# Performance work log

Hardware: AMD Instinct MI355X
Metric: run time of the kernel (lower is better)

Reference implementation:

```python
import jax, jax.numpy as jnp
import numpy as np

N_HEAD = 16
D_HEAD = 64
LN_EPS = 1e-5


def _layernorm(x, g, b):
    mu = jnp.mean(x, axis=-1, keepdims=True)
    var = jnp.mean((x - mu) ** 2, axis=-1, keepdims=True)
    return (x - mu) * jax.lax.rsqrt(var + LN_EPS) * g + b


def setup_inputs() -> dict:
    key = jax.random.key(0)
    ks = jax.random.split(key, 10)
    n_token, d_model, d_inner, n_layer = 32000, 1024, 4096, 6
    qlen, mlen, bsz = 512, 512, 4
    s = 0.02
    return {
        'data': jax.random.randint(ks[0], (qlen, bsz), 0, n_token),
        'mems': jax.random.normal(ks[1], (n_layer, mlen, bsz, d_model), jnp.float32) * s,
        'emb': jax.random.normal(ks[2], (n_token, d_model), jnp.float32) * s,
        'Wq': jax.random.normal(ks[3], (n_layer, d_model, N_HEAD * D_HEAD), jnp.float32) * s,
        'Wkv': jax.random.normal(ks[4], (n_layer, d_model, 2 * N_HEAD * D_HEAD), jnp.float32) * s,
        'Wo': jax.random.normal(ks[5], (n_layer, N_HEAD * D_HEAD, d_model), jnp.float32) * s,
        'ln1_g': jnp.ones((n_layer, d_model), jnp.float32),
        'ln1_b': jnp.zeros((n_layer, d_model), jnp.float32),
        'W1': jax.random.normal(ks[6], (n_layer, d_model, d_inner), jnp.float32) * s,
        'b1': jnp.zeros((n_layer, d_inner), jnp.float32),
        'W2': jax.random.normal(ks[7], (n_layer, d_inner, d_model), jnp.float32) * s,
        'b2': jnp.zeros((n_layer, d_model), jnp.float32),
        'ln2_g': jnp.ones((n_layer, d_model), jnp.float32),
        'ln2_b': jnp.zeros((n_layer, d_model), jnp.float32),
    }


def reference(data, mems, emb, Wq, Wkv, Wo, ln1_g, ln1_b, W1, b1, W2, b2, ln2_g, ln2_b):
    qlen, bsz = data.shape
    n_layer, _, d_model = Wo.shape
    mlen = mems.shape[1]
    klen = mlen + qlen
    scale = 1.0 / np.sqrt(D_HEAD)

    # AdaptiveEmbedding (div_val=1, d_proj==d_embed): lookup * sqrt(d_proj)
    word_emb = emb[data] * np.sqrt(d_model)  # [q, b, d]

    # sinusoidal positional embedding over klen (attn_type=2), last qlen slice
    inv_freq = 1.0 / (10000.0 ** (jnp.arange(0, d_model, 2, dtype=jnp.float32) / d_model))
    pos_seq = jnp.arange(klen - 1, -1, -1, dtype=jnp.float32)
    sinu = pos_seq[:, None] * inv_freq[None, :]
    pos_emb = jnp.concatenate([jnp.sin(sinu), jnp.cos(sinu)], axis=-1)  # [klen, d]
    h = word_emb + pos_emb[-qlen:, None, :]

    # causal mask including memory: True = masked
    mask = jnp.triu(jnp.ones((qlen, klen), dtype=bool), k=1 + mlen)

    for l in range(n_layer):
        c = jnp.concatenate([mems[l], h], axis=0)  # [klen, b, d]
        q = (h @ Wq[l]).reshape(qlen, bsz, N_HEAD, D_HEAD)
        kv = (c @ Wkv[l]).reshape(klen, bsz, N_HEAD, 2 * D_HEAD)
        k, v = kv[..., :D_HEAD], kv[..., D_HEAD:]
        score = jnp.einsum('ibnd,jbnd->ijbn', q, k) * scale  # [q, klen, b, n]
        score = jnp.where(mask[:, :, None, None], -jnp.inf, score)
        prob = jax.nn.softmax(score, axis=1)
        attn_vec = jnp.einsum('ijbn,jbnd->ibnd', prob, v).reshape(qlen, bsz, N_HEAD * D_HEAD)
        h = _layernorm(h + attn_vec @ Wo[l], ln1_g[l], ln1_b[l])  # post-LN
        ff = jax.nn.relu(h @ W1[l] + b1[l]) @ W2[l] + b2[l]
        h = _layernorm(h + ff, ln2_g[l], ln2_b[l])
    return h
```

## Files before the change

### kernel.cpp

```cpp
#include <hip/hip_runtime.h>

typedef unsigned short u16;
typedef unsigned int u32;
typedef __bf16 bf16x8 __attribute__((ext_vector_type(8)));
typedef float f32x4 __attribute__((ext_vector_type(4)));
typedef u16 u16x8 __attribute__((ext_vector_type(8)));
typedef u16 u16x4 __attribute__((ext_vector_type(4)));
typedef u32 u32x4 __attribute__((ext_vector_type(4)));

__device__ __forceinline__ u16 f2bf(float f){
  unsigned u = __float_as_uint(f);
  u += 0x7FFFu + ((u >> 16) & 1u);
  return (u16)(u >> 16);
}
__device__ __forceinline__ float bf2f(u16 u){
  return __uint_as_float((u32)u << 16);
}
__device__ __forceinline__ u32 pack2bf(float a, float b){
  return (u32)f2bf(a) | ((u32)f2bf(b) << 16);
}
__device__ __forceinline__ void gload16(const void* g, void* l){
  __builtin_amdgcn_global_load_lds(
      (const __attribute__((address_space(1))) void*)g,
      (__attribute__((address_space(3))) void*)l, 16, 0, 0);
}

__global__ __launch_bounds__(256) void conv_bf16_t(const float* __restrict__ src, u16* __restrict__ dst,
                                                   int K, int N, size_t dls, int drow0){
  __shared__ u16 s[64 * 68];
  size_t lo = (size_t)blockIdx.z * K * N;
  int n0 = blockIdx.x << 6, k0 = blockIdx.y << 6;
  int t = threadIdx.x;
#pragma unroll
  for (int p = 0; p < 4; ++p){
    int idx = p * 1024 + t * 4;
    int kl = idx >> 6, nl = idx & 63;
    f32x4 v = *(const f32x4*)(src + lo + (size_t)(k0 + kl) * N + n0 + nl);
#pragma unroll
    for (int j = 0; j < 4; ++j) s[(nl + j) * 68 + kl] = f2bf(v[j]);
  }
  __syncthreads();
  u16* db = dst + blockIdx.z * dls;
#pragma unroll
  for (int p = 0; p < 4; ++p){
    int idx = p * 1024 + t * 4;
    int nl = idx >> 6, kl = idx & 63;
    u16x4 o;
#pragma unroll
    for (int j = 0; j < 4; ++j) o[j] = s[nl * 68 + kl + j];
    *(u16x4*)(db + (size_t)(drow0 + n0 + nl) * K + k0 + kl) = o;
  }
}

__global__ __launch_bounds__(256) void conv_bf16(const float* __restrict__ src, u16* __restrict__ dst){
  size_t i = ((size_t)blockIdx.x * 256 + threadIdx.x) * 4;
  f32x4 v = *(const f32x4*)(src + i);
  u16x4 o;
#pragma unroll
  for (int j = 0; j < 4; ++j) o[j] = f2bf(v[j]);
  *(u16x4*)(dst + i) = o;
}

__global__ __launch_bounds__(256) void embed_k(const int* __restrict__ data, const float* __restrict__ emb,
                                               float* __restrict__ h, u16* __restrict__ hbf){
  int idx = blockIdx.x * 256 + threadIdx.x;
  int r = idx >> 10, d = idx & 1023;
  int i = r >> 2;
  int e = data[r];
  float val = emb[(size_t)e * 1024 + d] * 32.0f;
  float pos = (float)(511 - i);
  int t = d & 511;
  float freq = powf(10000.0f, -(float)t * (1.0f / 512.0f));
  float ang = pos * freq;
  val += (d < 512) ? sinf(ang) : cosf(ang);
  h[idx] = val;
  hbf[idx] = f2bf(val);
}

template<int BM>
__global__ __launch_bounds__(256) void gemm_bt(
    const u16* __restrict__ A, const u16* __restrict__ Bt,
    const float* __restrict__ bias, float* __restrict__ C, u16* __restrict__ Cbf,
    u16* __restrict__ Cpart, int M, int N, int K, int kchunk, int relu,
    size_t zA, size_t zB, size_t zC)
{
  constexpr int MFR = BM / 32;
  constexpr int ASZ = BM * 64, BSZ = 128 * 64;
  __shared__ __align__(16) u16 sA[2 * ASZ];
  __shared__ __align__(16) u16 sB[2 * BSZ];
  int tid = threadIdx.x, lane = tid & 63;
  int wr = (tid >> 7) & 1, wc = (tid >> 6) & 1;
  int m0 = blockIdx.y * BM, n0 = blockIdx.x << 7;
  int z = blockIdx.z;
  int kbeg = Cpart ? z * kchunk : 0;

  const u16* Ap = A + (size_t)z * zA;
  const u16* Bp = Bt + (size_t)z * zB;

  f32x4 acc[MFR][4];
#pragma unroll
  for (int i = 0; i < MFR; ++i)
#pragma unroll
    for (int j = 0; j < 4; ++j) acc[i][j] = (f32x4)(0.0f);

  int srow8 = tid >> 3;
  int gslot8 = ((tid & 7) ^ (srow8 & 7)) << 3;
  const u16* Ab = Ap + (size_t)(m0 + srow8) * K + kbeg + gslot8;
  const u16* Bb = Bp + (size_t)(n0 + srow8) * K + kbeg + gslot8;
  const size_t rstep32 = (size_t)K << 5;

  auto stage = [&](int buf, int k0){
#pragma unroll
    for (int p = 0; p < BM / 32; ++p)
      gload16(Ab + p * rstep32 + k0, (void*)&sA[buf * ASZ + p * 2048 + tid * 8]);
#pragma unroll
    for (int p = 0; p < 4; ++p)
      gload16(Bb + p * rstep32 + k0, (void*)&sB[buf * BSZ + p * 2048 + tid * 8]);
  };

  int r15 = lane & 15, g = lane >> 4;
  int s0 = g ^ (r15 & 7);
  const int o0 = s0 * 8, o1 = (s0 ^ 4) * 8;
  const int paBase = (wr * (BM / 2) + r15) * 64;
  const int pbBase = (wc * 64 + r15) * 64;

  int nk = kchunk >> 6;
  stage(0, 0);
  __syncthreads();
  for (int t = 0; t < nk; ++t){
    int cur = t & 1;
    if (t + 1 < nk) stage(cur ^ 1, (t + 1) << 6);
    const u16* pa = sA + cur * ASZ;
    const u16* pb = sB + cur * BSZ;
    bf16x8 af[MFR][2], bfv[4][2];
#pragma unroll
    for (int mi = 0; mi < MFR; ++mi){
      af[mi][0] = *(const bf16x8*)(pa + paBase + mi * 1024 + o0);
      af[mi][1] = *(const bf16x8*)(pa + paBase + mi * 1024 + o1);
    }
#pragma unroll
    for (int ni = 0; ni < 4; ++ni){
      bfv[ni][0] = *(const bf16x8*)(pb + pbBase + ni * 1024 + o0);
      bfv[ni][1] = *(const bf16x8*)(pb + pbBase + ni * 1024 + o1);
    }
#pragma unroll
    for (int kk = 0; kk < 2; ++kk)
#pragma unroll
      for (int mi = 0; mi < MFR; ++mi)
#pragma unroll
        for (int ni = 0; ni < 4; ++ni)
          acc[mi][ni] = __builtin_amdgcn_mfma_f32_16x16x32_bf16(af[mi][kk], bfv[ni][kk], acc[mi][ni], 0, 0, 0);
    __syncthreads();
  }

  int colf = lane & 15, rowf = (lane >> 4) << 2;
  if (Cpart){
    u16* dst = Cpart + (size_t)z * M * N;
#pragma unroll
    for (int ni = 0; ni < 4; ++ni){
      int cg = n0 + (wc << 6) + ni * 16 + colf;
#pragma unroll
      for (int mi = 0; mi < MFR; ++mi){
        int rg = m0 + wr * (BM / 2) + mi * 16 + rowf;
#pragma unroll
        for (int r = 0; r < 4; ++r)
          dst[(size_t)(rg + r) * N + cg] = f2bf(acc[mi][ni][r]);
      }
    }
  } else {
#pragma unroll
    for (int ni = 0; ni < 4; ++ni){
      int cg = n0 + (wc << 6) + ni * 16 + colf;
      float bv = bias ? bias[cg] : 0.0f;
#pragma unroll
      for (int mi = 0; mi < MFR; ++mi){
        int rg = m0 + wr * (BM / 2) + mi * 16 + rowf;
#pragma unroll
        for (int r = 0; r < 4; ++r){
          float val = acc[mi][ni][r] + bv;
          if (relu) val = fmaxf(val, 0.0f);
          size_t o = (size_t)(rg + r) * N + cg;
          if (C)   C[o]   = val;
          if (Cbf) (Cbf + (size_t)z * zC)[o] = f2bf(val);
        }
      }
    }
  }
}

__global__ __launch_bounds__(256) void vtrans(const u16* __restrict__ src, int sstride, int co,
                                              u16* __restrict__ dst, int jdst0,
                                              size_t zsrc, size_t zdst){
  __shared__ u16 s[64 * 68];
  int jt = blockIdx.x, bnp = blockIdx.y;
  int b = bnp >> 4, n = bnp & 15;
  int t = threadIdx.x;
  const u16* sp = src + blockIdx.z * zsrc;
  u16* dp = dst + blockIdx.z * zdst;
  int j0l = jt << 6;
#pragma unroll
  for (int rr = 0; rr < 16; ++rr){
    int idx = rr * 256 + t;
    int jl = idx >> 6, dd = idx & 63;
    s[jl * 68 + dd] = sp[(size_t)((j0l + jl) * 4 + b) * sstride + co + n * 128 + 64 + dd];
  }
  __syncthreads();
#pragma unroll
  for (int ww = 0; ww < 16; ++ww){
    int idx = ww * 256 + t;
    int dd = idx >> 6, jl = idx & 63;
    dp[((size_t)(bnp * 64 + dd) << 10) + jdst0 + j0l + jl] = s[jl * 68 + dd];
  }
}

__global__ __launch_bounds__(256) void attn_mfma_split(
    const u16* __restrict__ qkv, const u16* __restrict__ kvm,
    const u16* __restrict__ vtbf, u16* __restrict__ obuf, float* __restrict__ mlbuf)
{
  __shared__ __align__(16) u16 sK[2][64 * 64];
  __shared__ __align__(16) u16 sV[2][64 * 64];
  int tid = threadIdx.x, lane = tid & 63, wid = tid >> 6;
  int g = lane >> 4, t = lane & 15;
  int qt = blockIdx.x, bnp = blockIdx.y, half = blockIdx.z;
  int b = bnp >> 4, n = bnp & 15;
  int i0 = qt * 64 + wid * 16;
  int i = i0 + t;

  union Cvt { u32x4 u; bf16x8 v; };

  bf16x8 qfrag[2];
#pragma unroll
  for (int ks = 0; ks < 2; ++ks)
    qfrag[ks] = *(const bf16x8*)(qkv + (size_t)(i * 4 + b) * 3072 + n * 64 + ks * 32 + g * 8);

  f32x4 oacc[4];
#pragma unroll
  for (int df = 0; df < 4; ++df) oacc[df] = (f32x4)(0.0f);
  float mrun = -1e30f, lrun = 0.0f;

  const u16* kb2; size_t kst; int joff, kt0, kt1;
  if (half == 0){ kb2 = kvm + n * 128;        kst = 2048; joff = 0;   kt0 = 0; kt1 = 8; }
  else          { kb2 = qkv + 1024 + n * 128; kst = 3072; joff = 512; kt0 = 8; kt1 = qt + 9; }
  const u16* vb2 = vtbf + ((size_t)bnp << 16);

  int srow = tid >> 3;
  int gsl = ((tid & 7) ^ (srow & 7)) << 3;

  auto stageKV = [&](int buf, int kt){
    int j0 = kt << 6;
#pragma unroll
    for (int p = 0; p < 2; ++p){
      int jl = srow + p * 32;
      gload16(kb2 + (size_t)((j0 + jl - joff) * 4 + b) * kst + gsl, (void*)&sK[buf][p * 2048 + tid * 8]);
    }
#pragma unroll
    for (int p = 0; p < 2; ++p){
      int dl = srow + p * 32;
      gload16(vb2 + ((size_t)dl << 10) + j0 + gsl, (void*)&sV[buf][p * 2048 + tid * 8]);
    }
  };

  stageKV(0, kt0);
  __syncthreads();
  for (int kt = kt0; kt < kt1; ++kt){
    int cur = (kt - kt0) & 1;
    if (kt + 1 < kt1) stageKV(cur ^ 1, kt + 1);
    int j0 = kt << 6;
    f32x4 sacc[4];
#pragma unroll
    for (int jf = 0; jf < 4; ++jf) sacc[jf] = (f32x4)(0.0f);
#pragma unroll
    for (int ks = 0; ks < 2; ++ks){
      int sl = ((ks * 4 + g) ^ (t & 7)) * 8;
#pragma unroll
      for (int jf = 0; jf < 4; ++jf){
        bf16x8 kf = *(const bf16x8*)(&sK[cur][(jf * 16 + t) * 64 + sl]);
        sacc[jf] = __builtin_amdgcn_mfma_f32_16x16x32_bf16(kf, qfrag[ks], sacc[jf], 0, 0, 0);
      }
    }
    bool part = (half == 1) && (j0 + 63 > i0 + 512);
    float ps[4][4];
    float tmax = -1e30f;
#pragma unroll
    for (int jf = 0; jf < 4; ++jf)
#pragma unroll
      for (int r = 0; r < 4; ++r){
        float s = sacc[jf][r] * 0.125f;
        if (part && (j0 + jf * 16 + g * 4 + r > i + 512)) s = -1e30f;
        ps[jf][r] = s;
        tmax = fmaxf(tmax, s);
      }
    tmax = fmaxf(tmax, __shfl_xor(tmax, 16));
    tmax = fmaxf(tmax, __shfl_xor(tmax, 32));
    float mnew = fmaxf(mrun, tmax);
    float sc = __expf(mrun - mnew);
    mrun = mnew;
    lrun *= sc;
    u32 pk0[2], pk1[2], pk2[2], pk3[2];
    {
      float e0, e1, e2, e3;
#define DO_JF(PK, JF) \
      e0 = __expf(ps[JF][0] - mnew); e1 = __expf(ps[JF][1] - mnew); \
      e2 = __expf(ps[JF][2] - mnew); e3 = __expf(ps[JF][3] - mnew); \
      lrun += (e0 + e1) + (e2 + e3); \
      PK[0] = pack2bf(e0, e1); PK[1] = pack2bf(e2, e3);
      DO_JF(pk0, 0) DO_JF(pk1, 1) DO_JF(pk2, 2) DO_JF(pk3, 3)
#undef DO_JF
    }
#pragma unroll
    for (int df = 0; df < 4; ++df)
#pragma unroll
      for (int r = 0; r < 4; ++r) oacc[df][r] *= sc;

    int srcA = t + 16 * ((2 * g) & 3);
    int srcB = t + 16 * ((2 * g + 1) & 3);
    bool ghi = (g >= 2);
#pragma unroll
    for (int ks = 0; ks < 2; ++ks){
      u32 w0a, w1a, w2a, w3a, w0b, w1b, w2b, w3b;
      if (ks == 0){
        w0a = __shfl((int)pk0[0], srcA); w1a = __shfl((int)pk0[1], srcA);
        w2a = __shfl((int)pk0[0], srcB); w3a = __shfl((int)pk0[1], srcB);
        w0b = __shfl((int)pk1[0], srcA); w1b = __shfl((int)pk1[1], srcA);
        w2b = __shfl((int)pk1[0], srcB); w3b = __shfl((int)pk1[1], srcB);
      } else {
        w0a = __shfl((int)pk2[0], srcA); w1a = __shfl((int)pk2[1], srcA);
        w2a = __shfl((int)pk2[0], srcB); w3a = __shfl((int)pk2[1], srcB);
        w0b = __shfl((int)pk3[0], srcA); w1b = __shfl((int)pk3[1], srcA);
        w2b = __shfl((int)pk3[0], srcB); w3b = __shfl((int)pk3[1], srcB);
      }
      Cvt c;
      c.u[0] = ghi ? w0b : w0a;
      c.u[1] = ghi ? w1b : w1a;
      c.u[2] = ghi ? w2b : w2a;
      c.u[3] = ghi ? w3b : w3a;
      bf16x8 pf = c.v;
      int sl = ((ks * 4 + g) ^ (t & 7)) * 8;
#pragma unroll
      for (int df = 0; df < 4; ++df){
        bf16x8 vf = *(const bf16x8*)(&sV[cur][(df * 16 + t) * 64 + sl]);
        oacc[df] = __builtin_amdgcn_mfma_f32_16x16x32_bf16(vf, pf, oacc[df], 0, 0, 0);
      }
    }
    __syncthreads();
  }
  lrun += __shfl_xor(lrun, 16);
  lrun += __shfl_xor(lrun, 32);

  u16* orow = obuf + ((size_t)(half * 2048 + i * 4 + b) << 10) + n * 64;
#pragma unroll
  for (int df = 0; df < 4; ++df){
#pragma unroll
    for (int h = 0; h < 2; ++h){
      *(u32*)(orow + df * 16 + g * 4 + 2 * h) = pack2bf(oacc[df][2 * h], oacc[df][2 * h + 1]);
    }
  }
  if (g == 0){
    float* ml = mlbuf + (((size_t)(half * 2048 + i * 4 + b)) * 16 + n) * 2;
    ml[0] = mrun; ml[1] = lrun;
  }
}

__global__ __launch_bounds__(256) void attn_merge(const u16* __restrict__ obuf,
                                                  const float* __restrict__ mlbuf,
                                                  u16* __restrict__ attnbf){
  int r = blockIdx.x, tid = threadIdx.x;
  int d0 = tid * 4, n = tid >> 4;
  const float* ml0 = mlbuf + ((size_t)r * 16 + n) * 2;
  const float* ml1 = mlbuf + ((size_t)(2048 + r) * 16 + n) * 2;
  float m0 = ml0[0], l0 = ml0[1], m1 = ml1[0], l1 = ml1[1];
  float M = fmaxf(m0, m1);
  float w0 = __expf(m0 - M), w1 = __expf(m1 - M);
  float inv = 1.0f / (w0 * l0 + w1 * l1);
  u16x4 o0 = *(const u16x4*)(obuf + ((size_t)r << 10) + d0);
  u16x4 o1 = *(const u16x4*)(obuf + ((size_t)(2048 + r) << 10) + d0);
  u16x4 o;
#pragma unroll
  for (int j = 0; j < 4; ++j) o[j] = f2bf((w0 * bf2f(o0[j]) + w1 * bf2f(o1[j])) * inv);
  *(u16x4*)(attnbf + ((size_t)r << 10) + d0) = o;
}

__global__ __launch_bounds__(256) void ln_k(const float* __restrict__ res, const u16* __restrict__ parts,
                                            size_t pstride, int np, const float* __restrict__ bias,
                                            const float* __restrict__ g, const float* __restrict__ bta,
                                            float* hout, u16* __restrict__ hbf)
{
  int row = blockIdx.x, tid = threadIdx.x;
  int d0 = tid << 2;
  size_t ro = (size_t)row << 10;
  f32x4 v = *(const f32x4*)(res + ro + d0);
  if (bias){
    f32x4 bv = *(const f32x4*)(bias + d0);
#pragma unroll
    for (int j = 0; j < 4; ++j) v[j] += bv[j];
  }
  for (int p = 0; p < np; ++p){
    u16x4 pv = *(const u16x4*)(parts + p * pstride + ro + d0);
#pragma unroll
    for (int j = 0; j < 4; ++j) v[j] += bf2f(pv[j]);
  }
  float s = (v[0] + v[1]) + (v[2] + v[3]);
  float s2 = (v[0] * v[0] + v[1] * v[1]) + (v[2] * v[2] + v[3] * v[3]);
#pragma unroll
  for (int off = 32; off; off >>= 1){ s += __shfl_xor(s, off); s2 += __shfl_xor(s2, off); }
  __shared__ float ps[8];
  int wid = tid >> 6, lane = tid & 63;
  if (lane == 0){ ps[wid] = s; ps[wid + 4] = s2; }
  __syncthreads();
  s  = ps[0] + ps[1] + ps[2] + ps[3];
  s2 = ps[4] + ps[5] + ps[6] + ps[7];
  float mu = s * 0.0009765625f;
  float var = s2 * 0.0009765625f - mu * mu;
  float rstd = rsqrtf(var + 1e-5f);
  f32x4 gv = *(const f32x4*)(g + d0);
  f32x4 bt = *(const f32x4*)(bta + d0);
  f32x4 ho;
  u16x4 hb;
#pragma unroll
  for (int j = 0; j < 4; ++j){
    float tv = (v[j] - mu) * rstd * gv[j] + bt[j];
    ho[j] = tv; hb[j] = f2bf(tv);
  }
  *(f32x4*)(hout + ro + d0) = ho;
  *(u16x4*)(hbf + ro + d0) = hb;
}

__global__ __launch_bounds__(256) void copy_f32(const f32x4* __restrict__ src, f32x4* __restrict__ dst){
  size_t i = (size_t)blockIdx.x * 256 + threadIdx.x;
  dst[i] = src[i];
}

extern "C" void kernel_launch(void* const* d_in, const int* in_sizes, int n_in,
                              void* d_out, int out_size, void* d_ws, size_t ws_size,
                              hipStream_t stream)
{
  const int*   data = (const int*)  d_in[0];
  const float* mems = (const float*)d_in[1];
  const float* emb  = (const float*)d_in[2];
  const float* Wq   = (const float*)d_in[3];
  const float* Wkv  = (const float*)d_in[4];
  const float* Wo   = (const float*)d_in[5];
  const float* ln1g = (const float*)d_in[6];
  const float* ln1b = (const float*)d_in[7];
  const float* W1   = (const float*)d_in[8];
  const float* b1   = (const float*)d_in[9];
  const float* W2   = (const float*)d_in[10];
  const float* b2   = (const float*)d_in[11];
  const float* ln2g = (const float*)d_in[12];
  const float* ln2b = (const float*)d_in[13];
  float* out = (float*)d_out;

  char* ws = (char*)d_ws;
  size_t off = 0;
  auto alloc = [&](size_t bytes) -> char* {
    char* p = ws + off;
    off = (off + bytes + 255) & ~(size_t)255;
    return p;
  };

  u16*   wqkv_bf = (u16*) alloc((size_t)6 * 3072 * 1024 * 2);
  u16*   wo_bf   = (u16*) alloc((size_t)6 * 1024 * 1024 * 2);
  u16*   w1_bf   = (u16*) alloc((size_t)6 * 4096 * 1024 * 2);
  u16*   w2_bf   = (u16*) alloc((size_t)6 * 1024 * 4096 * 2);
  u16*   memsbf  = (u16*) alloc((size_t)6 * 2048 * 1024 * 2);
  u16*   kvmem   = (u16*) alloc((size_t)6 * 2048 * 2048 * 2);
  u16*   vtbf    = (u16*) alloc((size_t)6 * 64 * 64 * 1024 * 2);
  float* h       = (float*)alloc((size_t)2048 * 1024 * 4);
  u16*   hbf     = (u16*) alloc((size_t)2048 * 1024 * 2);
  u16*   qkv     = (u16*) alloc((size_t)2048 * 3072 * 2);
  u16*   attnbf  = (u16*) alloc((size_t)2048 * 1024 * 2);
  u16*   f1bf    = (u16*) alloc((size_t)2048 * 4096 * 2);
  float* pbuf    = (float*)alloc((size_t)4 * 2048 * 1024 * 4);
  float* mlbuf   = (float*)alloc((size_t)2 * 2048 * 16 * 2 * 4);
  u16*   pbf     = (u16*)pbuf;
  const size_t PS = (size_t)2048 * 1024;
  const size_t VTL = (size_t)64 * 64 * 1024;

  conv_bf16_t<<<dim3(16, 16, 6), 256, 0, stream>>>(Wq,  wqkv_bf, 1024, 1024, (size_t)3072 * 1024, 0);
  conv_bf16_t<<<dim3(32, 16, 6), 256, 0, stream>>>(Wkv, wqkv_bf, 1024, 2048, (size_t)3072 * 1024, 1024);
  conv_bf16_t<<<dim3(16, 16, 6), 256, 0, stream>>>(Wo,  wo_bf,   1024, 1024, (size_t)1024 * 1024, 0);
  conv_bf16_t<<<dim3(64, 16, 6), 256, 0, stream>>>(W1,  w1_bf,   1024, 4096, (size_t)4096 * 1024, 0);
  conv_bf16_t<<<dim3(16, 64, 6), 256, 0, stream>>>(W2,  w2_bf,   4096, 1024, (size_t)4096 * 1024, 0);
  conv_bf16<<<12288, 256, 0, stream>>>(mems, memsbf);
  embed_k<<<8192, 256, 0, stream>>>(data, emb, h, hbf);
  gemm_bt<128><<<dim3(16, 16, 6), 256, 0, stream>>>(memsbf, wqkv_bf + (size_t)1024 * 1024, nullptr,
      nullptr, kvmem, nullptr, 2048, 2048, 1024, 1024, 0,
      (size_t)2048 * 1024, (size_t)3072 * 1024, (size_t)2048 * 2048);
  vtrans<<<dim3(8, 64, 6), 256, 0, stream>>>(kvmem, 2048, 0, vtbf, 0, (size_t)2048 * 2048, VTL);

  for (int l = 0; l < 6; ++l){
    u16* kvm_l = kvmem + (size_t)l * 2048 * 2048;
    u16* vt_l  = vtbf + (size_t)l * VTL;
    gemm_bt<128><<<dim3(24, 16), 256, 0, stream>>>(hbf, wqkv_bf + (size_t)l * 3072 * 1024, nullptr,
        nullptr, qkv, nullptr, 2048, 3072, 1024, 1024, 0, 0, 0, 0);
    vtrans<<<dim3(8, 64), 256, 0, stream>>>(qkv, 3072, 1024, vt_l, 512, 0, 0);
    attn_mfma_split<<<dim3(8, 64, 2), 256, 0, stream>>>(qkv, kvm_l, vt_l, (u16*)pbuf, mlbuf);
    attn_merge<<<2048, 256, 0, stream>>>((const u16*)pbuf, mlbuf, attnbf);
    gemm_bt<64><<<dim3(8, 32, 2), 256, 0, stream>>>(attnbf, wo_bf + (size_t)l * 1024 * 1024, nullptr,
        nullptr, nullptr, pbf, 2048, 1024, 1024, 512, 0, 0, 0, 0);
    ln_k<<<2048, 256, 0, stream>>>(h, pbf, PS, 2, nullptr, ln1g + l * 1024, ln1b + l * 1024, h, hbf);
    gemm_bt<128><<<dim3(32, 16), 256, 0, stream>>>(hbf, w1_bf + (size_t)l * 4096 * 1024,
        b1 + (size_t)l * 4096, nullptr, f1bf, nullptr, 2048, 4096, 1024, 1024, 1, 0, 0, 0);
    gemm_bt<64><<<dim3(8, 32, 4), 256, 0, stream>>>(f1bf, w2_bf + (size_t)l * 4096 * 1024, nullptr,
        nullptr, nullptr, pbf, 2048, 1024, 4096, 1024, 0, 0, 0, 0);
    ln_k<<<2048, 256, 0, stream>>>(h, pbf, PS, 4, b2 + l * 1024, ln2g + l * 1024, ln2b + l * 1024, h, hbf);
  }
  copy_f32<<<2048, 256, 0, stream>>>((const f32x4*)h, (f32x4*)out);
}
```

Measured before the change: 1.189 ms.

## Unsplit attention into single pass and drop merge kernel; retile QKV GEMM

The attention kernel no longer splits the key range into a memory half and a current-segment half. Each block now walks all key tiles itself and normalizes the output directly, which removes the separate merge kernel and the intermediate partial-output and max/sum buffers. In exchange the grid halves to 512 blocks, so each block runs longer and fewer blocks are available to fill the GPU. The QKV projection GEMM also switches to the 64-row tile template with twice as many blocks.

```diff
diff --git a/kernel.cpp b/kernel.cpp
--- a/kernel.cpp
+++ b/kernel.cpp
@@ -213,15 +213,15 @@
   }
 }
 
-__global__ __launch_bounds__(256) void attn_mfma_split(
+__global__ __launch_bounds__(256) void attn_mfma(
     const u16* __restrict__ qkv, const u16* __restrict__ kvm,
-    const u16* __restrict__ vtbf, u16* __restrict__ obuf, float* __restrict__ mlbuf)
+    const u16* __restrict__ vtbf, u16* __restrict__ attnbf)
 {
   __shared__ __align__(16) u16 sK[2][64 * 64];
   __shared__ __align__(16) u16 sV[2][64 * 64];
   int tid = threadIdx.x, lane = tid & 63, wid = tid >> 6;
   int g = lane >> 4, t = lane & 15;
-  int qt = blockIdx.x, bnp = blockIdx.y, half = blockIdx.z;
+  int qt = blockIdx.x, bnp = blockIdx.y;
   int b = bnp >> 4, n = bnp & 15;
   int i0 = qt * 64 + wid * 16;
   int i = i0 + t;
@@ -238,9 +238,8 @@
   for (int df = 0; df < 4; ++df) oacc[df] = (f32x4)(0.0f);
   float mrun = -1e30f, lrun = 0.0f;
 
-  const u16* kb2; size_t kst; int joff, kt0, kt1;
-  if (half == 0){ kb2 = kvm + n * 128;        kst = 2048; joff = 0;   kt0 = 0; kt1 = 8; }
-  else          { kb2 = qkv + 1024 + n * 128; kst = 3072; joff = 512; kt0 = 8; kt1 = qt + 9; }
+  const u16* kbm = kvm + n * 128;
+  const u16* kbh = qkv + 1024 + n * 128;
   const u16* vb2 = vtbf + ((size_t)bnp << 16);
 
   int srow = tid >> 3;
@@ -248,10 +247,13 @@
 
   auto stageKV = [&](int buf, int kt){
     int j0 = kt << 6;
+    const u16* kb = (kt < 8) ? kbm : kbh;
+    size_t kst = (kt < 8) ? 2048 : 3072;
+    int joff = (kt < 8) ? 0 : 512;
 #pragma unroll
     for (int p = 0; p < 2; ++p){
       int jl = srow + p * 32;
-      gload16(kb2 + (size_t)((j0 + jl - joff) * 4 + b) * kst + gsl, (void*)&sK[buf][p * 2048 + tid * 8]);
+      gload16(kb + (size_t)((j0 + jl - joff) * 4 + b) * kst + gsl, (void*)&sK[buf][p * 2048 + tid * 8]);
     }
 #pragma unroll
     for (int p = 0; p < 2; ++p){
@@ -260,10 +262,11 @@
     }
   };
 
-  stageKV(0, kt0);
+  int kt1 = qt + 9;
+  stageKV(0, 0);
   __syncthreads();
-  for (int kt = kt0; kt < kt1; ++kt){
-    int cur = (kt - kt0) & 1;
+  for (int kt = 0; kt < kt1; ++kt){
+    int cur = kt & 1;
     if (kt + 1 < kt1) stageKV(cur ^ 1, kt + 1);
     int j0 = kt << 6;
     f32x4 sacc[4];
@@ -278,7 +281,7 @@
         sacc[jf] = __builtin_amdgcn_mfma_f32_16x16x32_bf16(kf, qfrag[ks], sacc[jf], 0, 0, 0);
       }
     }
-    bool part = (half == 1) && (j0 + 63 > i0 + 512);
+    bool part = (j0 + 63 > i0 + 512);
     float ps[4][4];
     float tmax = -1e30f;
 #pragma unroll
@@ -346,38 +349,16 @@
   }
   lrun += __shfl_xor(lrun, 16);
   lrun += __shfl_xor(lrun, 32);
-
-  u16* orow = obuf + ((size_t)(half * 2048 + i * 4 + b) << 10) + n * 64;
+  float inv = 1.0f / lrun;
+
+  u16* orow = attnbf + ((size_t)(i * 4 + b) << 10) + n * 64;
 #pragma unroll
   for (int df = 0; df < 4; ++df){
 #pragma unroll
     for (int h = 0; h < 2; ++h){
-      *(u32*)(orow + df * 16 + g * 4 + 2 * h) = pack2bf(oacc[df][2 * h], oacc[df][2 * h + 1]);
-    }
-  }
-  if (g == 0){
-    float* ml = mlbuf + (((size_t)(half * 2048 + i * 4 + b)) * 16 + n) * 2;
-    ml[0] = mrun; ml[1] = lrun;
-  }
-}
-
-__global__ __launch_bounds__(256) void attn_merge(const u16* __restrict__ obuf,
-                                                  const float* __restrict__ mlbuf,
-                                                  u16* __restrict__ attnbf){
-  int r = blockIdx.x, tid = threadIdx.x;
-  int d0 = tid * 4, n = tid >> 4;
-  const float* ml0 = mlbuf + ((size_t)r * 16 + n) * 2;
-  const float* ml1 = mlbuf + ((size_t)(2048 + r) * 16 + n) * 2;
-  float m0 = ml0[0], l0 = ml0[1], m1 = ml1[0], l1 = ml1[1];
-  float M = fmaxf(m0, m1);
-  float w0 = __expf(m0 - M), w1 = __expf(m1 - M);
-  float inv = 1.0f / (w0 * l0 + w1 * l1);
-  u16x4 o0 = *(const u16x4*)(obuf + ((size_t)r << 10) + d0);
-  u16x4 o1 = *(const u16x4*)(obuf + ((size_t)(2048 + r) << 10) + d0);
-  u16x4 o;
-#pragma unroll
-  for (int j = 0; j < 4; ++j) o[j] = f2bf((w0 * bf2f(o0[j]) + w1 * bf2f(o1[j])) * inv);
-  *(u16x4*)(attnbf + ((size_t)r << 10) + d0) = o;
+      *(u32*)(orow + df * 16 + g * 4 + 2 * h) = pack2bf(oacc[df][2 * h] * inv, oacc[df][2 * h + 1] * inv);
+    }
+  }
 }
 
 __global__ __launch_bounds__(256) void ln_k(const float* __restrict__ res, const u16* __restrict__ parts,
@@ -470,9 +451,7 @@
   u16*   qkv     = (u16*) alloc((size_t)2048 * 3072 * 2);
   u16*   attnbf  = (u16*) alloc((size_t)2048 * 1024 * 2);
   u16*   f1bf    = (u16*) alloc((size_t)2048 * 4096 * 2);
-  float* pbuf    = (float*)alloc((size_t)4 * 2048 * 1024 * 4);
-  float* mlbuf   = (float*)alloc((size_t)2 * 2048 * 16 * 2 * 4);
-  u16*   pbf     = (u16*)pbuf;
+  u16*   pbf     = (u16*) alloc((size_t)4 * 2048 * 1024 * 2);
   const size_t PS = (size_t)2048 * 1024;
   const size_t VTL = (size_t)64 * 64 * 1024;
 
@@ -491,11 +470,10 @@
   for (int l = 0; l < 6; ++l){
     u16* kvm_l = kvmem + (size_t)l * 2048 * 2048;
     u16* vt_l  = vtbf + (size_t)l * VTL;
-    gemm_bt<128><<<dim3(24, 16), 256, 0, stream>>>(hbf, wqkv_bf + (size_t)l * 3072 * 1024, nullptr,
+    gemm_bt<64><<<dim3(24, 32), 256, 0, stream>>>(hbf, wqkv_bf + (size_t)l * 3072 * 1024, nullptr,
         nullptr, qkv, nullptr, 2048, 3072, 1024, 1024, 0, 0, 0, 0);
     vtrans<<<dim3(8, 64), 256, 0, stream>>>(qkv, 3072, 1024, vt_l, 512, 0, 0);
-    attn_mfma_split<<<dim3(8, 64, 2), 256, 0, stream>>>(qkv, kvm_l, vt_l, (u16*)pbuf, mlbuf);
-    attn_merge<<<2048, 256, 0, stream>>>((const u16*)pbuf, mlbuf, attnbf);
+    attn_mfma<<<dim3(8, 64), 256, 0, stream>>>(qkv, kvm_l, vt_l, attnbf);
     gemm_bt<64><<<dim3(8, 32, 2), 256, 0, stream>>>(attnbf, wo_bf + (size_t)l * 1024 * 1024, nullptr,
         nullptr, nullptr, pbf, 2048, 1024, 1024, 512, 0, 0, 0, 0);
     ln_k<<<2048, 256, 0, stream>>>(h, pbf, PS, 2, nullptr, ln1g + l * 1024, ln1b + l * 1024, h, hbf);
```

New measurement: 1.169 ms. Within noise of the previous version (-1.7%).
